# Performance work log

Measured on AMD Instinct MI355X. Metric: run time of the kernel, lower is better.

The kernel has to match this reference:

```python
import jax, jax.numpy as jnp
import numpy as np

B_SZ, L, D_MODEL = 2, 1024, 1024
D_INNER, D_STATE, D_CONV = 2048, 16, 4
EPS = 1e-6


def setup_inputs() -> dict:
    key = jax.random.key(0)
    ks = jax.random.split(key, 8)
    def n(k, shape, scale=0.02):
        return jax.random.normal(k, shape, jnp.float32) * scale
    return {
        "x": jax.random.normal(ks[0], (B_SZ, L, D_MODEL), jnp.float32),
        "W_in": n(ks[1], (D_MODEL, 2 * D_INNER)),
        "b_in": jnp.zeros((2 * D_INNER,), jnp.float32),
        "conv_w": n(ks[2], (D_INNER, 1, D_CONV), 0.2),
        "conv_b": jnp.zeros((D_INNER,), jnp.float32),
        "W_xp": n(ks[3], (D_INNER, 2 * D_STATE)),
        "b_xp": jnp.zeros((2 * D_STATE,), jnp.float32),
        "W_dt": n(ks[4], (D_INNER, D_INNER)),
        "b_dt": jnp.full((D_INNER,), -1.0, jnp.float32),
        # torch code does log(randn) (NaN-prone); use log of positive uniform instead
        "A_log": jnp.log(jax.random.uniform(ks[5], (D_INNER, D_STATE), jnp.float32, 0.5, 1.5)),
        "D_skip": jnp.ones((D_INNER,), jnp.float32),
        "W_out": n(ks[6], (D_INNER, D_MODEL)),
        "b_out": jnp.zeros((D_MODEL,), jnp.float32),
        "alpha": jnp.ones((D_MODEL,), jnp.float32),
        "beta": jnp.zeros((D_MODEL,), jnp.float32),
    }


def _selective_scan(xc, delta, A, Bm, Cm, D_skip):
    # xc, delta: (B,L,di); A: (di,ds); Bm, Cm: (B,L,ds)
    dA = jnp.exp(delta[..., None] * A)                     # (B,L,di,ds)
    dBx = (delta * xc)[..., None] * Bm[:, :, None, :]      # (B,L,di,ds)
    h0 = jnp.zeros((xc.shape[0], xc.shape[2], A.shape[1]), xc.dtype)

    def step(h, inp):
        dA_t, dBx_t, C_t = inp
        h = dA_t * h + dBx_t                               # (B,di,ds)
        y_t = jnp.einsum('bds,bs->bd', h, C_t)
        return h, y_t

    _, ys = jax.lax.scan(
        step, h0,
        (dA.transpose(1, 0, 2, 3), dBx.transpose(1, 0, 2, 3), Cm.transpose(1, 0, 2)))
    y = ys.transpose(1, 0, 2)                              # (B,L,di)
    return y + D_skip * xc


def _layernorm(r, alpha, beta):
    # torch LayerNormalization: unbiased std, eps added to std
    mean = jnp.mean(r, axis=-1, keepdims=True)
    diff = r - mean
    var_unb = jnp.sum(diff * diff, axis=-1, keepdims=True) / (r.shape[-1] - 1)
    std = jnp.sqrt(var_unb)
    return alpha * diff / (std + EPS) + beta


def reference(x, W_in, b_in, conv_w, conv_b, W_xp, b_xp, W_dt, b_dt,
              A_log, D_skip, W_out, b_out, alpha, beta):
    residual = x
    xz = x @ W_in + b_in                                   # (B,L,2*di)
    x_in, z = jnp.split(xz, 2, axis=-1)

    # depthwise causal conv1d (torch pads d_conv-1 both sides, slices [:L])
    xt = x_in.transpose(0, 2, 1)                           # (B,di,L)
    xt = jax.lax.conv_general_dilated(
        xt, conv_w, window_strides=(1,), padding=[(D_CONV - 1, 0)],
        feature_group_count=D_INNER, dimension_numbers=('NCH', 'OIH', 'NCH'))
    xt = xt + conv_b[None, :, None]
    x_conv = jax.nn.silu(xt.transpose(0, 2, 1))            # (B,L,di)

    x_proj_out = x_conv @ W_xp + b_xp                      # (B,L,2*ds)
    Bm, Cm = jnp.split(x_proj_out, 2, axis=-1)
    delta = jax.nn.softplus(x_conv @ W_dt + b_dt)          # (B,L,di)
    A = -jnp.exp(A_log)

    y = _selective_scan(x_conv, delta, A, Bm, Cm, D_skip)
    y = y * jax.nn.silu(z)
    out = y @ W_out + b_out                                # (B,L,D)
    return _layernorm(residual + out, alpha, beta)
```

## Files before the change

kernel.cpp:

```cpp
#include <hip/hip_runtime.h>
#include <math.h>

#define B_SZ    2
#define L_SEQ   1024
#define DMODEL  1024
#define DINNER  2048
#define DSTATE  16
#define EPSV    1e-6f

#define CCH 32
#define CS  (L_SEQ / CCH)
#define DT  16

typedef short  bf16x8  __attribute__((ext_vector_type(8)));
typedef float  floatx4 __attribute__((ext_vector_type(4)));
typedef unsigned short ushort8v __attribute__((ext_vector_type(8)));

__device__ __forceinline__ unsigned short f2bf(float f) {
    unsigned int u = __float_as_uint(f);
    unsigned int r = (u + 0x7FFFu + ((u >> 16) & 1u)) >> 16;
    return (unsigned short)r;
}

__global__ __launch_bounds__(256) void cast_bf16_kernel(
    const float* __restrict__ in, unsigned short* __restrict__ out, int n4)
{
    int i = blockIdx.x * 256 + threadIdx.x;
    if (i >= n4) return;
    float4 v = ((const float4*)in)[i];
    ushort4 o = { f2bf(v.x), f2bf(v.y), f2bf(v.z), f2bf(v.w) };
    ((ushort4*)out)[i] = o;
}

__global__ __launch_bounds__(256) void transpose_cast(
    const float* __restrict__ W, unsigned short* __restrict__ Wt, int K, int N)
{
    __shared__ float tile[32][33];
    const int n0 = blockIdx.x * 32;
    const int k0 = blockIdx.y * 32;
    const int c = threadIdx.x & 31;
    const int r = threadIdx.x >> 5;
#pragma unroll
    for (int i = 0; i < 4; ++i)
        tile[r + 8 * i][c] = W[(size_t)(k0 + r + 8 * i) * N + n0 + c];
    __syncthreads();
#pragma unroll
    for (int i = 0; i < 4; ++i)
        Wt[(size_t)(n0 + r + 8 * i) * K + k0 + c] = f2bf(tile[c][r + 8 * i]);
}

template <int TM, int TN, int MODE>
__global__ __launch_bounds__(256, 3) void gemm_bf16(
    const unsigned short* __restrict__ A, const unsigned short* __restrict__ Bt,
    const float* __restrict__ bias, const float* __restrict__ resid,
    float* __restrict__ C, int M, int N, int K)
{
    constexpr int MI = TM / 32;
    constexpr int NJ = TN / 32;
    constexpr int NLOAD = (TM + TN) / 32;

    __shared__ unsigned short As[TM * 64];
    __shared__ unsigned short Bs[TN * 64];

    const int tid  = threadIdx.x;
    const int wave = tid >> 6;
    const int lane = tid & 63;
    const int m0 = blockIdx.y * TM;
    const int n0 = blockIdx.x * TN;
    const int wm = (wave >> 1) * (TM / 2);
    const int wn = (wave & 1) * (TN / 2);
    const int fr = lane & 15;
    const int kg = lane >> 4;

    int offs[NLOAD];
    unsigned short* lp[NLOAD];
#pragma unroll
    for (int i = 0; i < NLOAD; ++i) {
        const int slot = i * 256 + tid;
        const int row  = slot >> 3;
        const int ch   = slot & 7;
        const int pos  = ch ^ (row & 7);
        if (i < TM / 32) {
            offs[i] = (m0 + row) * K + ch * 8;
            lp[i]   = &As[row * 64 + pos * 8];
        } else {
            const int rb = row - TM;
            offs[i] = (n0 + rb) * K + ch * 8;
            lp[i]   = &Bs[rb * 64 + pos * 8];
        }
    }

    floatx4 acc[MI][NJ] = {};
    bf16x8 pre[NLOAD];

#pragma unroll
    for (int i = 0; i < NLOAD; ++i)
        pre[i] = *(const bf16x8*)((i < TM / 32 ? A : Bt) + offs[i]);
#pragma unroll
    for (int i = 0; i < NLOAD; ++i)
        *(bf16x8*)lp[i] = pre[i];
    __syncthreads();

    for (int kt = 0; kt < K; kt += 64) {
        const bool more = (kt + 64) < K;
        if (more) {
#pragma unroll
            for (int i = 0; i < NLOAD; ++i)
                pre[i] = *(const bf16x8*)((i < TM / 32 ? A : Bt) + offs[i] + kt + 64);
        }

#pragma unroll
        for (int ks = 0; ks < 2; ++ks) {
            const int cq = (ks << 2) | kg;
            bf16x8 af[MI], bfv[NJ];
#pragma unroll
            for (int i = 0; i < MI; ++i) {
                const int row = wm + i * 16 + fr;
                af[i] = *(const bf16x8*)&As[row * 64 + ((cq ^ (row & 7)) << 3)];
            }
#pragma unroll
            for (int j = 0; j < NJ; ++j) {
                const int row = wn + j * 16 + fr;
                bfv[j] = *(const bf16x8*)&Bs[row * 64 + ((cq ^ (row & 7)) << 3)];
            }
#pragma unroll
            for (int i = 0; i < MI; ++i)
#pragma unroll
                for (int j = 0; j < NJ; ++j)
                    acc[i][j] = __builtin_amdgcn_mfma_f32_16x16x32_bf16(
                        af[i], bfv[j], acc[i][j], 0, 0, 0);
        }
        __syncthreads();
        if (more) {
#pragma unroll
            for (int i = 0; i < NLOAD; ++i)
                *(bf16x8*)lp[i] = pre[i];
        }
        __syncthreads();
    }

    const int rq = (lane >> 4) * 4;
#pragma unroll
    for (int i = 0; i < MI; ++i) {
#pragma unroll
        for (int j = 0; j < NJ; ++j) {
            const int col = n0 + wn + j * 16 + fr;
            const float bv = bias[col];
#pragma unroll
            for (int r = 0; r < 4; ++r) {
                const int row = m0 + wm + i * 16 + rq + r;
                float v = acc[i][j][r] + bv;
                if (MODE == 1) {
                    v = (v > 20.f) ? v : log1pf(__expf(v));
                } else if (MODE == 2) {
                    v += resid[(size_t)row * N + col];
                }
                C[(size_t)row * N + col] = v;
            }
        }
    }
}

#define CROWS 4
__global__ __launch_bounds__(256) void conv_xproj(
    const float* __restrict__ xz, const float* __restrict__ conv_w,
    const float* __restrict__ conv_b, const float* __restrict__ W_xp,
    const float* __restrict__ b_xp, float* __restrict__ x_conv,
    unsigned short* __restrict__ x_conv_bf, float* __restrict__ BC)
{
    __shared__ float sxc[CROWS][DINNER];
    __shared__ float red[8][CROWS][32];

    const int tid = threadIdx.x;
    const int r0 = blockIdx.x * CROWS;
    const int c8 = tid * 8;

    float wt[8][4];
#pragma unroll
    for (int ci = 0; ci < 8; ++ci) {
        float4 w4 = *(const float4*)&conv_w[(c8 + ci) * 4];
        wt[ci][0] = w4.x; wt[ci][1] = w4.y; wt[ci][2] = w4.z; wt[ci][3] = w4.w;
    }
    float cb[8];
    *(float4*)&cb[0] = *(const float4*)&conv_b[c8];
    *(float4*)&cb[4] = *(const float4*)&conv_b[c8 + 4];

#pragma unroll
    for (int rr = 0; rr < CROWS; ++rr) {
        const int row = r0 + rr;
        const int l = row & (L_SEQ - 1);
        float acc[8];
#pragma unroll
        for (int ci = 0; ci < 8; ++ci) acc[ci] = cb[ci];
#pragma unroll
        for (int h = 0; h < 4; ++h) {
            const int lsrc = l - 3 + h;
            if (lsrc >= 0) {
                float4 a = *(const float4*)&xz[(size_t)(row - 3 + h) * (2 * DINNER) + c8];
                float4 b = *(const float4*)&xz[(size_t)(row - 3 + h) * (2 * DINNER) + c8 + 4];
                acc[0] += a.x * wt[0][h]; acc[1] += a.y * wt[1][h];
                acc[2] += a.z * wt[2][h]; acc[3] += a.w * wt[3][h];
                acc[4] += b.x * wt[4][h]; acc[5] += b.y * wt[5][h];
                acc[6] += b.z * wt[6][h]; acc[7] += b.w * wt[7][h];
            }
        }
        float o[8];
        ushort8v ob;
#pragma unroll
        for (int ci = 0; ci < 8; ++ci) {
            o[ci] = acc[ci] / (1.f + __expf(-acc[ci]));
            sxc[rr][c8 + ci] = o[ci];
            ob[ci] = (short)f2bf(o[ci]);
        }
        *(float4*)&x_conv[(size_t)row * DINNER + c8]     = *(float4*)&o[0];
        *(float4*)&x_conv[(size_t)row * DINNER + c8 + 4] = *(float4*)&o[4];
        *(ushort8v*)&x_conv_bf[(size_t)row * DINNER + c8] = ob;
    }
    __syncthreads();

    const int n = tid & 31;
    const int g = tid >> 5;
    float p[CROWS] = {};
    const int k0 = g * 256;
#pragma unroll 4
    for (int k = k0; k < k0 + 256; ++k) {
        const float wv = W_xp[k * 32 + n];
        p[0] += sxc[0][k] * wv;
        p[1] += sxc[1][k] * wv;
        p[2] += sxc[2][k] * wv;
        p[3] += sxc[3][k] * wv;
    }
#pragma unroll
    for (int rr = 0; rr < CROWS; ++rr) red[g][rr][n] = p[rr];
    __syncthreads();
    if (tid < CROWS * 32) {
        const int rr = tid >> 5;
        const int n2 = tid & 31;
        float s = b_xp[n2];
#pragma unroll
        for (int gg = 0; gg < 8; ++gg) s += red[gg][rr][n2];
        BC[(size_t)(r0 + rr) * 32 + n2] = s;
    }
}

__global__ __launch_bounds__(512) void scan_kernel(
    const float* __restrict__ delta, const float* __restrict__ x_conv,
    const float* __restrict__ BC, const float* __restrict__ A_log,
    const float* __restrict__ D_skip, const float* __restrict__ xz,
    unsigned short* __restrict__ y_bf)
{
    __shared__ float sA[DSTATE][CCH][DT];
    __shared__ float sH[DSTATE][CCH][DT];

    const int tid = threadIdx.x;
    const int dl  = tid & (DT - 1);
    const int c   = tid >> 4;
    const int b   = blockIdx.x >> 7;
    const int d0  = (blockIdx.x & 127) * DT;
    const int d   = d0 + dl;

    float Al[DSTATE];
#pragma unroll
    for (int s = 0; s < DSTATE; ++s)
        Al[s] = -__expf(A_log[d * DSTATE + s]) * 1.44269504f;
    const float Dsk = D_skip[d];

    float h[DSTATE];
#pragma unroll
    for (int s = 0; s < DSTATE; ++s) h[s] = 0.f;
    float dsum = 0.f;
    const int l0 = c * CS;

    for (int j = 0; j < CS; ++j) {
        const size_t r = (size_t)(b * L_SEQ + l0 + j);
        const float dt = delta[r * DINNER + d];
        const float xc = x_conv[r * DINNER + d];
        float Bv[DSTATE];
        *(float4*)&Bv[0]  = *(const float4*)&BC[r * 32 + 0];
        *(float4*)&Bv[4]  = *(const float4*)&BC[r * 32 + 4];
        *(float4*)&Bv[8]  = *(const float4*)&BC[r * 32 + 8];
        *(float4*)&Bv[12] = *(const float4*)&BC[r * 32 + 12];
        dsum += dt;
        const float dlx = dt * xc;
#pragma unroll
        for (int s = 0; s < DSTATE; ++s) {
            const float e = exp2f(dt * Al[s]);
            h[s] = e * h[s] + dlx * Bv[s];
        }
    }
#pragma unroll
    for (int s = 0; s < DSTATE; ++s) {
        sH[s][c][dl] = h[s];
        sA[s][c][dl] = exp2f(Al[s] * dsum);
    }
    __syncthreads();

    if (tid < DSTATE * DT) {
        const int dl2 = tid & (DT - 1);
        const int s2  = tid >> 4;
        float hh = 0.f;
#pragma unroll
        for (int c2 = 0; c2 < CCH; ++c2) {
            const float a  = sA[s2][c2][dl2];
            const float he = sH[s2][c2][dl2];
            sH[s2][c2][dl2] = hh;
            hh = a * hh + he;
        }
    }
    __syncthreads();

#pragma unroll
    for (int s = 0; s < DSTATE; ++s) h[s] = sH[s][c][dl];

    for (int j = 0; j < CS; ++j) {
        const size_t r = (size_t)(b * L_SEQ + l0 + j);
        const float dt = delta[r * DINNER + d];
        const float xc = x_conv[r * DINNER + d];
        const float z  = xz[r * (2 * DINNER) + DINNER + d];
        float Bv[DSTATE], Cv[DSTATE];
        *(float4*)&Bv[0]  = *(const float4*)&BC[r * 32 + 0];
        *(float4*)&Bv[4]  = *(const float4*)&BC[r * 32 + 4];
        *(float4*)&Bv[8]  = *(const float4*)&BC[r * 32 + 8];
        *(float4*)&Bv[12] = *(const float4*)&BC[r * 32 + 12];
        *(float4*)&Cv[0]  = *(const float4*)&BC[r * 32 + 16];
        *(float4*)&Cv[4]  = *(const float4*)&BC[r * 32 + 20];
        *(float4*)&Cv[8]  = *(const float4*)&BC[r * 32 + 24];
        *(float4*)&Cv[12] = *(const float4*)&BC[r * 32 + 28];
        const float dlx = dt * xc;
        float y = Dsk * xc;
#pragma unroll
        for (int s = 0; s < DSTATE; ++s) {
            const float e = exp2f(dt * Al[s]);
            h[s] = e * h[s] + dlx * Bv[s];
            y += h[s] * Cv[s];
        }
        const float g = z / (1.f + __expf(-z));
        y_bf[r * DINNER + d] = f2bf(y * g);
    }
}

__global__ __launch_bounds__(256) void layernorm_kernel(
    const float* __restrict__ t, const float* __restrict__ alpha,
    const float* __restrict__ beta, float* __restrict__ out)
{
    __shared__ float sred[4];
    __shared__ float sred2[4];
    const int row = blockIdx.x;
    const int tid = threadIdx.x;
    const float* r = t + (size_t)row * DMODEL;

    float4 v = *(const float4*)&r[tid * 4];
    float lsum = v.x + v.y + v.z + v.w;
#pragma unroll
    for (int m = 1; m < 64; m <<= 1) lsum += __shfl_xor(lsum, m);
    if ((tid & 63) == 0) sred[tid >> 6] = lsum;
    __syncthreads();
    const float mean = (sred[0] + sred[1] + sred[2] + sred[3]) * (1.f / DMODEL);

    const float dx = v.x - mean, dy = v.y - mean, dz = v.z - mean, dw = v.w - mean;
    float ls2 = dx * dx + dy * dy + dz * dz + dw * dw;
#pragma unroll
    for (int m = 1; m < 64; m <<= 1) ls2 += __shfl_xor(ls2, m);
    if ((tid & 63) == 0) sred2[tid >> 6] = ls2;
    __syncthreads();
    const float var = (sred2[0] + sred2[1] + sred2[2] + sred2[3]) * (1.f / (DMODEL - 1));
    const float inv = 1.f / (sqrtf(var) + EPSV);

    float4 a4 = *(const float4*)&alpha[tid * 4];
    float4 b4 = *(const float4*)&beta[tid * 4];
    float4 o;
    o.x = a4.x * dx * inv + b4.x;
    o.y = a4.y * dy * inv + b4.y;
    o.z = a4.z * dz * inv + b4.z;
    o.w = a4.w * dw * inv + b4.w;
    *(float4*)&out[(size_t)row * DMODEL + tid * 4] = o;
}

extern "C" void kernel_launch(void* const* d_in, const int* in_sizes, int n_in,
                              void* d_out, int out_size, void* d_ws, size_t ws_size,
                              hipStream_t stream)
{
    const float* x      = (const float*)d_in[0];
    const float* W_in   = (const float*)d_in[1];
    const float* b_in   = (const float*)d_in[2];
    const float* conv_w = (const float*)d_in[3];
    const float* conv_b = (const float*)d_in[4];
    const float* W_xp   = (const float*)d_in[5];
    const float* b_xp   = (const float*)d_in[6];
    const float* W_dt   = (const float*)d_in[7];
    const float* b_dt   = (const float*)d_in[8];
    const float* A_log  = (const float*)d_in[9];
    const float* D_skip = (const float*)d_in[10];
    const float* W_out  = (const float*)d_in[11];
    const float* b_out  = (const float*)d_in[12];
    const float* alpha  = (const float*)d_in[13];
    const float* beta   = (const float*)d_in[14];
    float* out = (float*)d_out;

    const size_t M = (size_t)B_SZ * L_SEQ;
    char* ws = (char*)d_ws;
    float* xz      = (float*)(ws + 0);
    float* x_conv  = (float*)(ws + (32u << 20));
    float* delta   = (float*)(ws + (48u << 20));
    float* BC      = (float*)(ws + (64u << 20));
    unsigned short* x_bf       = (unsigned short*)(ws + (64u << 20) + (512u << 10));
    unsigned short* W_in_t     = (unsigned short*)(ws + (69u << 20));
    unsigned short* W_dt_t     = (unsigned short*)(ws + (77u << 20));
    unsigned short* W_out_t    = (unsigned short*)(ws + (85u << 20));
    unsigned short* x_conv_bf  = (unsigned short*)(ws + (89u << 20));
    unsigned short* ygate_bf   = (unsigned short*)(ws + (77u << 20));
    float* tpre = xz;

    const dim3 blk(256);

    cast_bf16_kernel<<<dim3((unsigned)(M * DMODEL / 4 / 256)), blk, 0, stream>>>(
        x, x_bf, (int)(M * DMODEL / 4));
    transpose_cast<<<dim3(2 * DINNER / 32, DMODEL / 32), blk, 0, stream>>>(
        W_in, W_in_t, DMODEL, 2 * DINNER);
    transpose_cast<<<dim3(DINNER / 32, DINNER / 32), blk, 0, stream>>>(
        W_dt, W_dt_t, DINNER, DINNER);
    transpose_cast<<<dim3(DMODEL / 32, DINNER / 32), blk, 0, stream>>>(
        W_out, W_out_t, DINNER, DMODEL);

    gemm_bf16<128, 64, 0><<<dim3(4096 / 64, 2048 / 128), blk, 0, stream>>>(
        x_bf, W_in_t, b_in, nullptr, xz, 2048, 4096, 1024);

    conv_xproj<<<dim3((unsigned)(M / CROWS)), blk, 0, stream>>>(
        xz, conv_w, conv_b, W_xp, b_xp, x_conv, x_conv_bf, BC);

    gemm_bf16<128, 64, 1><<<dim3(2048 / 64, 2048 / 128), blk, 0, stream>>>(
        x_conv_bf, W_dt_t, b_dt, nullptr, delta, 2048, 2048, 2048);

    scan_kernel<<<dim3(B_SZ * (DINNER / DT)), dim3(512), 0, stream>>>(
        delta, x_conv, BC, A_log, D_skip, xz, ygate_bf);

    gemm_bf16<64, 64, 2><<<dim3(1024 / 64, 2048 / 64), blk, 0, stream>>>(
        ygate_bf, W_out_t, b_out, x, tpre, 2048, 1024, 2048);

    layernorm_kernel<<<dim3((unsigned)M), blk, 0, stream>>>(tpre, alpha, beta, out);
}
```

Before: 299.3 us.

## Store delta and x_conv in bf16 for scan; double scan chunks to 64

The delta GEMM now writes softplus output as bf16, and conv_xproj no longer writes an fp32 x_conv. The scan reads bf16 delta and x_conv, which roughly halves the bytes it loads for those two streams and removes a large fp32 write. The scan block grows to 1024 threads with 64 chunks of 16 steps, and the shared state arrays get a padded stride. The loops are unrolled by 2. The cost is lower precision for delta and x_conv inside the recurrence and a longer serial cross-chunk combine.

```diff
diff --git a/kernel.cpp b/kernel.cpp
--- a/kernel.cpp
+++ b/kernel.cpp
@@ -8,9 +8,10 @@
 #define DSTATE  16
 #define EPSV    1e-6f
 
-#define CCH 32
+#define CCH 64
 #define CS  (L_SEQ / CCH)
 #define DT  16
+#define SSTR (CCH * DT + 1)
 
 typedef short  bf16x8  __attribute__((ext_vector_type(8)));
 typedef float  floatx4 __attribute__((ext_vector_type(4)));
@@ -20,6 +21,9 @@
     unsigned int u = __float_as_uint(f);
     unsigned int r = (u + 0x7FFFu + ((u >> 16) & 1u)) >> 16;
     return (unsigned short)r;
+}
+__device__ __forceinline__ float bf2f(unsigned short u) {
+    return __uint_as_float(((unsigned int)u) << 16);
 }
 
 __global__ __launch_bounds__(256) void cast_bf16_kernel(
@@ -150,12 +154,15 @@
             for (int r = 0; r < 4; ++r) {
                 const int row = m0 + wm + i * 16 + rq + r;
                 float v = acc[i][j][r] + bv;
-                if (MODE == 1) {
+                if (MODE == 1 || MODE == 3) {
                     v = (v > 20.f) ? v : log1pf(__expf(v));
                 } else if (MODE == 2) {
                     v += resid[(size_t)row * N + col];
                 }
-                C[(size_t)row * N + col] = v;
+                if (MODE == 3)
+                    ((unsigned short*)C)[(size_t)row * N + col] = f2bf(v);
+                else
+                    C[(size_t)row * N + col] = v;
             }
         }
     }
@@ -165,7 +172,7 @@
 __global__ __launch_bounds__(256) void conv_xproj(
     const float* __restrict__ xz, const float* __restrict__ conv_w,
     const float* __restrict__ conv_b, const float* __restrict__ W_xp,
-    const float* __restrict__ b_xp, float* __restrict__ x_conv,
+    const float* __restrict__ b_xp,
     unsigned short* __restrict__ x_conv_bf, float* __restrict__ BC)
 {
     __shared__ float sxc[CROWS][DINNER];
@@ -212,8 +219,6 @@
             sxc[rr][c8 + ci] = o[ci];
             ob[ci] = (short)f2bf(o[ci]);
         }
-        *(float4*)&x_conv[(size_t)row * DINNER + c8]     = *(float4*)&o[0];
-        *(float4*)&x_conv[(size_t)row * DINNER + c8 + 4] = *(float4*)&o[4];
         *(ushort8v*)&x_conv_bf[(size_t)row * DINNER + c8] = ob;
     }
     __syncthreads();
@@ -243,14 +248,15 @@
     }
 }
 
-__global__ __launch_bounds__(512) void scan_kernel(
-    const float* __restrict__ delta, const float* __restrict__ x_conv,
+__global__ __launch_bounds__(1024) void scan_kernel(
+    const unsigned short* __restrict__ delta_bf,
+    const unsigned short* __restrict__ xc_bf,
     const float* __restrict__ BC, const float* __restrict__ A_log,
     const float* __restrict__ D_skip, const float* __restrict__ xz,
     unsigned short* __restrict__ y_bf)
 {
-    __shared__ float sA[DSTATE][CCH][DT];
-    __shared__ float sH[DSTATE][CCH][DT];
+    __shared__ float sA[DSTATE * SSTR];
+    __shared__ float sH[DSTATE * SSTR];
 
     const int tid = threadIdx.x;
     const int dl  = tid & (DT - 1);
@@ -270,11 +276,13 @@
     for (int s = 0; s < DSTATE; ++s) h[s] = 0.f;
     float dsum = 0.f;
     const int l0 = c * CS;
-
+    const size_t row0 = (size_t)(b * L_SEQ + l0);
+
+#pragma unroll 2
     for (int j = 0; j < CS; ++j) {
-        const size_t r = (size_t)(b * L_SEQ + l0 + j);
-        const float dt = delta[r * DINNER + d];
-        const float xc = x_conv[r * DINNER + d];
+        const size_t r = row0 + j;
+        const float dt = bf2f(delta_bf[r * DINNER + d]);
+        const float xc = bf2f(xc_bf[r * DINNER + d]);
         float Bv[DSTATE];
         *(float4*)&Bv[0]  = *(const float4*)&BC[r * 32 + 0];
         *(float4*)&Bv[4]  = *(const float4*)&BC[r * 32 + 4];
@@ -290,8 +298,8 @@
     }
 #pragma unroll
     for (int s = 0; s < DSTATE; ++s) {
-        sH[s][c][dl] = h[s];
-        sA[s][c][dl] = exp2f(Al[s] * dsum);
+        sH[s * SSTR + c * DT + dl] = h[s];
+        sA[s * SSTR + c * DT + dl] = exp2f(Al[s] * dsum);
     }
     __syncthreads();
 
@@ -301,21 +309,23 @@
         float hh = 0.f;
 #pragma unroll
         for (int c2 = 0; c2 < CCH; ++c2) {
-            const float a  = sA[s2][c2][dl2];
-            const float he = sH[s2][c2][dl2];
-            sH[s2][c2][dl2] = hh;
+            const int idx = s2 * SSTR + c2 * DT + dl2;
+            const float a  = sA[idx];
+            const float he = sH[idx];
+            sH[idx] = hh;
             hh = a * hh + he;
         }
     }
     __syncthreads();
 
 #pragma unroll
-    for (int s = 0; s < DSTATE; ++s) h[s] = sH[s][c][dl];
-
+    for (int s = 0; s < DSTATE; ++s) h[s] = sH[s * SSTR + c * DT + dl];
+
+#pragma unroll 2
     for (int j = 0; j < CS; ++j) {
-        const size_t r = (size_t)(b * L_SEQ + l0 + j);
-        const float dt = delta[r * DINNER + d];
-        const float xc = x_conv[r * DINNER + d];
+        const size_t r = row0 + j;
+        const float dt = bf2f(delta_bf[r * DINNER + d]);
+        const float xc = bf2f(xc_bf[r * DINNER + d]);
         const float z  = xz[r * (2 * DINNER) + DINNER + d];
         float Bv[DSTATE], Cv[DSTATE];
         *(float4*)&Bv[0]  = *(const float4*)&BC[r * 32 + 0];
@@ -400,8 +410,7 @@
     const size_t M = (size_t)B_SZ * L_SEQ;
     char* ws = (char*)d_ws;
     float* xz      = (float*)(ws + 0);
-    float* x_conv  = (float*)(ws + (32u << 20));
-    float* delta   = (float*)(ws + (48u << 20));
+    unsigned short* delta_bf = (unsigned short*)(ws + (48u << 20));
     float* BC      = (float*)(ws + (64u << 20));
     unsigned short* x_bf       = (unsigned short*)(ws + (64u << 20) + (512u << 10));
     unsigned short* W_in_t     = (unsigned short*)(ws + (69u << 20));
@@ -426,13 +435,13 @@
         x_bf, W_in_t, b_in, nullptr, xz, 2048, 4096, 1024);
 
     conv_xproj<<<dim3((unsigned)(M / CROWS)), blk, 0, stream>>>(
-        xz, conv_w, conv_b, W_xp, b_xp, x_conv, x_conv_bf, BC);
-
-    gemm_bf16<128, 64, 1><<<dim3(2048 / 64, 2048 / 128), blk, 0, stream>>>(
-        x_conv_bf, W_dt_t, b_dt, nullptr, delta, 2048, 2048, 2048);
-
-    scan_kernel<<<dim3(B_SZ * (DINNER / DT)), dim3(512), 0, stream>>>(
-        delta, x_conv, BC, A_log, D_skip, xz, ygate_bf);
+        xz, conv_w, conv_b, W_xp, b_xp, x_conv_bf, BC);
+
+    gemm_bf16<128, 64, 3><<<dim3(2048 / 64, 2048 / 128), blk, 0, stream>>>(
+        x_conv_bf, W_dt_t, b_dt, nullptr, (float*)delta_bf, 2048, 2048, 2048);
+
+    scan_kernel<<<dim3(B_SZ * (DINNER / DT)), dim3(1024), 0, stream>>>(
+        delta_bf, x_conv_bf, BC, A_log, D_skip, xz, ygate_bf);
 
     gemm_bf16<64, 64, 2><<<dim3(1024 / 64, 2048 / 64), blk, 0, stream>>>(
         ygate_bf, W_out_t, b_out, x, tpre, 2048, 1024, 2048);
```

Result: no change. 299.8 us (+0.2%).
